# Kernel tuning notes

Hardware: AMD Instinct MI355X
Metric: run time of the kernel (lower is better)

The kernel has to match this reference:

```python
import jax, jax.numpy as jnp
import numpy as np


def setup_inputs() -> dict:
    key = jax.random.key(0)
    k1, k2 = jax.random.split(key)
    x = jax.random.normal(k1, (32, 64, 64, 64), dtype=jnp.float32)
    codebook = jax.random.normal(k2, (1024, 64), dtype=jnp.float32)
    return {"x": x, "codebook": codebook}


def reference(x, codebook):
    # x: (B, D, H, W)  codebook: (K, D)
    B, D = x.shape[0], x.shape[1]
    spatial = x.shape[2:]
    flat = x.reshape(B, D, -1).transpose(0, 2, 1)  # (B, N, D)
    dot = jnp.einsum("bnd,kd->bnk", flat, codebook)
    cb_norm = jnp.sum(codebook * codebook, axis=-1)  # (K,)
    indices = jnp.argmin(cb_norm[None, None, :] - 2.0 * dot, axis=-1)  # (B, N)
    quantized = codebook[indices]  # (B, N, D) gather
    out = quantized.transpose(0, 2, 1).reshape(x.shape)
    return out, indices.reshape((B,) + spatial)
```

## Files before the change

### kernel.cpp

```cpp
#include <hip/hip_runtime.h>


typedef _Float16 f16x8 __attribute__((ext_vector_type(8)));
typedef float    f32x4 __attribute__((ext_vector_type(4)));

#define VQ_D    64
#define VQ_HW   4096
#define VQ_NPOS 131072
#define SC      2048.0f
#define ISC     (1.0f / 2048.0f)
#define EPS     2.0e-3f
#define WS_CBN  65536
#define WS_CBT  66560
#define WS_CNT  132096
#define WS_LIST 132100

__global__ __launch_bounds__(256)
void vq_prep(const float* __restrict__ cb, float* __restrict__ ws)
{
    const int tid = threadIdx.x;
    const int blk = blockIdx.x;
    if (blk < 64) {
        const int it   = blk * 256 + tid;
        const int ct   = it >> 8;
        const int s    = (it >> 6) & 3;
        const int lane = it & 63;
        const int ks   = s & 1, isR = s >> 1;
        const int n    = ct * 16 + (lane & 15);
        const int k0   = ks * 32 + (lane >> 4) * 8;
        const float* src = cb + n * 64 + k0;
        f16x8 o;
        #pragma unroll
        for (int j = 0; j < 8; ++j) {
            const float b = src[j];
            const _Float16 bh = (_Float16)b;
            o[j] = isR ? (_Float16)((b - (float)bh) * (-2.0f * SC))
                       : (_Float16)(-2.0f * (float)bh);
        }
        ((f16x8*)ws)[it] = o;
    } else if (blk < 128) {
        const int it = (blk - 64) * 256 + tid;
        const int k = it >> 4, j4 = it & 15;
        ((float4*)(ws + WS_CBT))[j4 * 1024 + k] = ((const float4*)cb)[it];
    } else {
        const int k = (blk - 128) * 256 + tid;
        const float4* row = (const float4*)(cb + k * 64);
        float a0 = 0.f, a1 = 0.f, a2 = 0.f, a3 = 0.f;
        #pragma unroll
        for (int j = 0; j < 16; ++j) {
            const float4 c = row[j];
            a0 = fmaf(c.x, c.x, a0); a1 = fmaf(c.y, c.y, a1);
            a2 = fmaf(c.z, c.z, a2); a3 = fmaf(c.w, c.w, a3);
        }
        ws[WS_CBN + k] = (a0 + a1) + (a2 + a3);
        if (k == 0) ((int*)ws)[WS_CNT] = 0;
    }
}

#define PREFETCH(B0, B1, R0, R1, CV, CTN)                          \
    {                                                              \
        const f16x8* base_ = bp + (CTN) * 256;                     \
        B0 = base_[lane];       B1 = base_[64 + lane];             \
        R0 = base_[128 + lane]; R1 = base_[192 + lane];            \
        CV = cnb[(CTN) * 16 + m];                                  \
    }

#define COMPUTE(B0, B1, R0, R1, CV, CTV)                                                   \
    {                                                                                      \
        const f32x4 Ci = {CV, CV, CV, CV};                                                 \
        f32x4 acm[4], acc[4];                                                              \
        _Pragma("unroll")                                                                  \
        for (int tl = 0; tl < 4; ++tl) {                                                   \
            acm[tl] = __builtin_amdgcn_mfma_f32_16x16x32_f16(Ah[tl][0], B0, Ci,      0,0,0);\
            acm[tl] = __builtin_amdgcn_mfma_f32_16x16x32_f16(Ah[tl][1], B1, acm[tl], 0,0,0);\
            acc[tl] = __builtin_amdgcn_mfma_f32_16x16x32_f16(Ah[tl][0], R0, zero4,   0,0,0);\
            acc[tl] = __builtin_amdgcn_mfma_f32_16x16x32_f16(Ah[tl][1], R1, acc[tl], 0,0,0);\
            acc[tl] = __builtin_amdgcn_mfma_f32_16x16x32_f16(Ra[tl][0], B0, acc[tl], 0,0,0);\
            acc[tl] = __builtin_amdgcn_mfma_f32_16x16x32_f16(Ra[tl][1], B1, acc[tl], 0,0,0);\
        }                                                                                  \
        const int code_ = (CTV) * 16 + m;                                                  \
        _Pragma("unroll")                                                                  \
        for (int tl = 0; tl < 4; ++tl)                                                     \
            _Pragma("unroll")                                                              \
            for (int r = 0; r < 4; ++r) {                                                  \
                const float dist = fmaf(acc[tl][r], ISC, acm[tl][r]);                      \
                const float od   = d1[tl][r];                                              \
                const bool  c    = dist < od;                                              \
                d2[tl][r] = __builtin_amdgcn_fmed3f(dist, od, d2[tl][r]);                  \
                d1[tl][r] = c ? dist : od;                                                 \
                k1[tl][r] = c ? code_ : k1[tl][r];                                         \
            }                                                                              \
    }

__global__ __launch_bounds__(256, 2)
void vq_main(const float* __restrict__ x,
             const float* __restrict__ cb,
             float* __restrict__ ws,
             float* __restrict__ out,
             float* __restrict__ idx_out)
{
    __shared__ int   sk[256];
    __shared__ float smg[256];

    const int tid  = threadIdx.x;
    const int lane = tid & 63;
    const int wv   = tid >> 6;
    const int m    = lane & 15;
    const int q    = lane >> 4;

    const f16x8* bp  = (const f16x8*)ws;
    const float* cnb = ws + WS_CBN;

    const int p0 = blockIdx.x * 256;
    const int b  = p0 >> 12;
    const int n0 = p0 & (VQ_HW - 1);
    const float* xw = x + (size_t)b * (VQ_D * VQ_HW) + n0 + wv * 64;

    f16x8 Ah[4][2], Ra[4][2];
    #pragma unroll
    for (int tl = 0; tl < 4; ++tl)
        #pragma unroll
        for (int ks = 0; ks < 2; ++ks) {
            f16x8 h8, r8;
            #pragma unroll
            for (int j = 0; j < 8; ++j) {
                const int k = ks * 32 + q * 8 + j;
                const float v = xw[(size_t)k * VQ_HW + tl * 16 + m];
                const _Float16 vh = (_Float16)v;
                h8[j] = vh;
                r8[j] = (_Float16)((v - (float)vh) * SC);
            }
            Ah[tl][ks] = h8; Ra[tl][ks] = r8;
        }

    float d1[4][4], d2[4][4]; int k1[4][4];
    #pragma unroll
    for (int tl = 0; tl < 4; ++tl)
        #pragma unroll
        for (int r = 0; r < 4; ++r) { d1[tl][r] = 3.4e38f; d2[tl][r] = 3.4e38f; k1[tl][r] = 0; }

    const f32x4 zero4 = {0.f, 0.f, 0.f, 0.f};

    f16x8 B0a, B1a, R0a, R1a, B0b, B1b, R0b, R1b;
    float cva, cvb;
    PREFETCH(B0a, B1a, R0a, R1a, cva, 0)
    PREFETCH(B0b, B1b, R0b, R1b, cvb, 1)

    for (int ct = 0; ct < 64; ct += 2) {
        COMPUTE(B0a, B1a, R0a, R1a, cva, ct)
        {
            const int ctn = (ct + 2 < 64) ? ct + 2 : 62;
            PREFETCH(B0a, B1a, R0a, R1a, cva, ctn)
        }
        COMPUTE(B0b, B1b, R0b, R1b, cvb, ct + 1)
        {
            const int ctn = (ct + 3 < 64) ? ct + 3 : 63;
            PREFETCH(B0b, B1b, R0b, R1b, cvb, ctn)
        }
    }

    #pragma unroll
    for (int off = 1; off < 16; off <<= 1)
        #pragma unroll
        for (int tl = 0; tl < 4; ++tl)
            #pragma unroll
            for (int r = 0; r < 4; ++r) {
                const float od1 = __shfl_xor(d1[tl][r], off, 64);
                const float od2 = __shfl_xor(d2[tl][r], off, 64);
                const int   ok1 = __shfl_xor(k1[tl][r], off, 64);
                const float nd2 = fminf(fmaxf(d1[tl][r], od1), fminf(d2[tl][r], od2));
                const bool  sw  = (od1 < d1[tl][r]) ||
                                  (od1 == d1[tl][r] && ok1 < k1[tl][r]);
                d1[tl][r] = sw ? od1 : d1[tl][r];
                k1[tl][r] = sw ? ok1 : k1[tl][r];
                d2[tl][r] = nd2;
            }

    if (m == 0) {
        #pragma unroll
        for (int tl = 0; tl < 4; ++tl)
            #pragma unroll
            for (int r = 0; r < 4; ++r) {
                const int li = wv * 64 + tl * 16 + q * 4 + r;
                sk[li]  = k1[tl][r];
                smg[li] = d2[tl][r] - d1[tl][r];
            }
    }
    __syncthreads();

    idx_out[p0 + tid] = (float)sk[tid];
    if (smg[tid] < EPS) {
        const int slot = atomicAdd((int*)ws + WS_CNT, 1);
        ((int*)ws)[WS_LIST + slot] = p0 + tid;
    }
    const int bk = sk[tid];
    const float4* cr = (const float4*)(cb + (size_t)bk * VQ_D);
    float* ob = out + (size_t)b * (VQ_D * VQ_HW) + n0 + tid;
    #pragma unroll
    for (int d4 = 0; d4 < 16; ++d4) {
        const float4 v = cr[d4];
        ob[(size_t)(d4 * 4 + 0) * VQ_HW] = v.x;
        ob[(size_t)(d4 * 4 + 1) * VQ_HW] = v.y;
        ob[(size_t)(d4 * 4 + 2) * VQ_HW] = v.z;
        ob[(size_t)(d4 * 4 + 3) * VQ_HW] = v.w;
    }
}

__global__ __launch_bounds__(64)
void vq_rescan(const float* __restrict__ x,
               const float* __restrict__ cb,
               const float* __restrict__ ws,
               float* __restrict__ out,
               float* __restrict__ idx_out)
{
    __shared__ float xs[VQ_D];
    const int lane = threadIdx.x;
    const int cnt  = ((const int*)ws)[WS_CNT];
    const int* list = (const int*)ws + WS_LIST;
    const float*  cnb  = ws + WS_CBN;
    const float4* cbT4 = (const float4*)(ws + WS_CBT);

    for (int i = blockIdx.x; i < cnt; i += gridDim.x) {
        const int p = list[i];
        const int b = p >> 12, n = p & (VQ_HW - 1);
        xs[lane] = x[(size_t)b * (VQ_D * VQ_HW) + (size_t)lane * VQ_HW + n];
        __syncthreads();
        float4 xr[16];
        #pragma unroll
        for (int j = 0; j < 16; ++j) xr[j] = ((const float4*)xs)[j];

        float bd = 3.4e38f; int bk = 0;
        #pragma unroll 4
        for (int t = 0; t < 16; ++t) {
            const int code = t * 64 + lane;
            float a0 = 0.f, a1 = 0.f, a2 = 0.f, a3 = 0.f;
            #pragma unroll
            for (int j4 = 0; j4 < 16; ++j4) {
                const float4 c = cbT4[j4 * 1024 + code];
                a0 = fmaf(xr[j4].x, c.x, a0); a1 = fmaf(xr[j4].y, c.y, a1);
                a2 = fmaf(xr[j4].z, c.z, a2); a3 = fmaf(xr[j4].w, c.w, a3);
            }
            const float dist = fmaf(-2.0f, (a0 + a1) + (a2 + a3), cnb[code]);
            if (dist < bd) { bd = dist; bk = code; }
        }
        #pragma unroll
        for (int off = 1; off < 64; off <<= 1) {
            const float od = __shfl_xor(bd, off, 64);
            const int   ok = __shfl_xor(bk, off, 64);
            if (od < bd || (od == bd && ok < bk)) { bd = od; bk = ok; }
        }
        out[(size_t)b * (VQ_D * VQ_HW) + (size_t)lane * VQ_HW + n] = cb[(size_t)bk * VQ_D + lane];
        if (lane == 0) idx_out[p] = (float)bk;
        __syncthreads();
    }
}

extern "C" void kernel_launch(void* const* d_in, const int* in_sizes, int n_in,
                              void* d_out, int out_size, void* d_ws, size_t ws_size,
                              hipStream_t stream) {
    const float* x  = (const float*)d_in[0];
    const float* cb = (const float*)d_in[1];
    float* out = (float*)d_out;
    float* idx = out + (size_t)VQ_NPOS * VQ_D;
    float* ws  = (float*)d_ws;

    vq_prep  <<<dim3(132),  dim3(256), 0, stream>>>(cb, ws);
    vq_main  <<<dim3(512),  dim3(256), 0, stream>>>(x, cb, ws, out, idx);
    vq_rescan<<<dim3(1024), dim3(64),  0, stream>>>(x, cb, ws, out, idx);
}
```

Before: 162.4 us.

## Use single fp16 MFMA pass with packed index, LDS-staged codebook, wider rescan

Drops the split-fp16 residual MFMAs, so the main kernel computes distances with one fp16 product per codebook tile. The code index is packed into the low mantissa bits so argmin reduces to plain fminf. Codebook tiles are staged through double-buffered LDS, and blocks shrink to 128 positions with higher occupancy. The looser approximation is covered by raising the rescan margin from 2e-3 to 1.0 and launching more rescan blocks, which risks many more positions falling to the slow exact rescan.

```diff
diff --git a/kernel.cpp b/kernel.cpp
--- a/kernel.cpp
+++ b/kernel.cpp
@@ -7,9 +7,7 @@
 #define VQ_D    64
 #define VQ_HW   4096
 #define VQ_NPOS 131072
-#define SC      2048.0f
-#define ISC     (1.0f / 2048.0f)
-#define EPS     2.0e-3f
+#define EPS     1.0f
 #define WS_CBN  65536
 #define WS_CBT  66560
 #define WS_CNT  132096
@@ -20,30 +18,25 @@
 {
     const int tid = threadIdx.x;
     const int blk = blockIdx.x;
-    if (blk < 64) {
+    if (blk < 32) {
         const int it   = blk * 256 + tid;
-        const int ct   = it >> 8;
-        const int s    = (it >> 6) & 3;
+        const int ct   = it >> 7;
+        const int s    = (it >> 6) & 1;
         const int lane = it & 63;
-        const int ks   = s & 1, isR = s >> 1;
         const int n    = ct * 16 + (lane & 15);
-        const int k0   = ks * 32 + (lane >> 4) * 8;
+        const int k0   = s * 32 + (lane >> 4) * 8;
         const float* src = cb + n * 64 + k0;
         f16x8 o;
         #pragma unroll
-        for (int j = 0; j < 8; ++j) {
-            const float b = src[j];
-            const _Float16 bh = (_Float16)b;
-            o[j] = isR ? (_Float16)((b - (float)bh) * (-2.0f * SC))
-                       : (_Float16)(-2.0f * (float)bh);
-        }
+        for (int j = 0; j < 8; ++j)
+            o[j] = (_Float16)(-2.0f * (float)(_Float16)src[j]);
         ((f16x8*)ws)[it] = o;
-    } else if (blk < 128) {
-        const int it = (blk - 64) * 256 + tid;
+    } else if (blk < 96) {
+        const int it = (blk - 32) * 256 + tid;
         const int k = it >> 4, j4 = it & 15;
         ((float4*)(ws + WS_CBT))[j4 * 1024 + k] = ((const float4*)cb)[it];
     } else {
-        const int k = (blk - 128) * 256 + tid;
+        const int k = (blk - 96) * 256 + tid;
         const float4* row = (const float4*)(cb + k * 64);
         float a0 = 0.f, a1 = 0.f, a2 = 0.f, a3 = 0.f;
         #pragma unroll
@@ -57,50 +50,17 @@
     }
 }
 
-#define PREFETCH(B0, B1, R0, R1, CV, CTN)                          \
-    {                                                              \
-        const f16x8* base_ = bp + (CTN) * 256;                     \
-        B0 = base_[lane];       B1 = base_[64 + lane];             \
-        R0 = base_[128 + lane]; R1 = base_[192 + lane];            \
-        CV = cnb[(CTN) * 16 + m];                                  \
-    }
-
-#define COMPUTE(B0, B1, R0, R1, CV, CTV)                                                   \
-    {                                                                                      \
-        const f32x4 Ci = {CV, CV, CV, CV};                                                 \
-        f32x4 acm[4], acc[4];                                                              \
-        _Pragma("unroll")                                                                  \
-        for (int tl = 0; tl < 4; ++tl) {                                                   \
-            acm[tl] = __builtin_amdgcn_mfma_f32_16x16x32_f16(Ah[tl][0], B0, Ci,      0,0,0);\
-            acm[tl] = __builtin_amdgcn_mfma_f32_16x16x32_f16(Ah[tl][1], B1, acm[tl], 0,0,0);\
-            acc[tl] = __builtin_amdgcn_mfma_f32_16x16x32_f16(Ah[tl][0], R0, zero4,   0,0,0);\
-            acc[tl] = __builtin_amdgcn_mfma_f32_16x16x32_f16(Ah[tl][1], R1, acc[tl], 0,0,0);\
-            acc[tl] = __builtin_amdgcn_mfma_f32_16x16x32_f16(Ra[tl][0], B0, acc[tl], 0,0,0);\
-            acc[tl] = __builtin_amdgcn_mfma_f32_16x16x32_f16(Ra[tl][1], B1, acc[tl], 0,0,0);\
-        }                                                                                  \
-        const int code_ = (CTV) * 16 + m;                                                  \
-        _Pragma("unroll")                                                                  \
-        for (int tl = 0; tl < 4; ++tl)                                                     \
-            _Pragma("unroll")                                                              \
-            for (int r = 0; r < 4; ++r) {                                                  \
-                const float dist = fmaf(acc[tl][r], ISC, acm[tl][r]);                      \
-                const float od   = d1[tl][r];                                              \
-                const bool  c    = dist < od;                                              \
-                d2[tl][r] = __builtin_amdgcn_fmed3f(dist, od, d2[tl][r]);                  \
-                d1[tl][r] = c ? dist : od;                                                 \
-                k1[tl][r] = c ? code_ : k1[tl][r];                                         \
-            }                                                                              \
-    }
-
-__global__ __launch_bounds__(256, 2)
+__global__ __launch_bounds__(256, 4)
 void vq_main(const float* __restrict__ x,
              const float* __restrict__ cb,
              float* __restrict__ ws,
              float* __restrict__ out,
              float* __restrict__ idx_out)
 {
-    __shared__ int   sk[256];
-    __shared__ float smg[256];
+    __shared__ f16x8 bbuf[2][1024];
+    __shared__ float cn_lds[1024];
+    __shared__ int   sk[128];
+    __shared__ float smg[128];
 
     const int tid  = threadIdx.x;
     const int lane = tid & 63;
@@ -108,96 +68,113 @@
     const int m    = lane & 15;
     const int q    = lane >> 4;
 
-    const f16x8* bp  = (const f16x8*)ws;
-    const float* cnb = ws + WS_CBN;
-
-    const int p0 = blockIdx.x * 256;
+    const int p0 = blockIdx.x * 128;
     const int b  = p0 >> 12;
     const int n0 = p0 & (VQ_HW - 1);
-    const float* xw = x + (size_t)b * (VQ_D * VQ_HW) + n0 + wv * 64;
-
-    f16x8 Ah[4][2], Ra[4][2];
-    #pragma unroll
-    for (int tl = 0; tl < 4; ++tl)
+    const float* xw = x + (size_t)b * (VQ_D * VQ_HW) + n0 + wv * 32;
+
+    ((float4*)cn_lds)[tid] = ((const float4*)(ws + WS_CBN))[tid];
+
+    const float4* g0 = (const float4*)ws;
+    float4 u0 = g0[tid], u1 = g0[256 + tid], u2 = g0[512 + tid], u3 = g0[768 + tid];
+
+    f16x8 Ah[2][2];
+    #pragma unroll
+    for (int tl = 0; tl < 2; ++tl)
         #pragma unroll
         for (int ks = 0; ks < 2; ++ks) {
-            f16x8 h8, r8;
-            #pragma unroll
-            for (int j = 0; j < 8; ++j) {
-                const int k = ks * 32 + q * 8 + j;
-                const float v = xw[(size_t)k * VQ_HW + tl * 16 + m];
-                const _Float16 vh = (_Float16)v;
-                h8[j] = vh;
-                r8[j] = (_Float16)((v - (float)vh) * SC);
-            }
-            Ah[tl][ks] = h8; Ra[tl][ks] = r8;
-        }
-
-    float d1[4][4], d2[4][4]; int k1[4][4];
-    #pragma unroll
-    for (int tl = 0; tl < 4; ++tl)
-        #pragma unroll
-        for (int r = 0; r < 4; ++r) { d1[tl][r] = 3.4e38f; d2[tl][r] = 3.4e38f; k1[tl][r] = 0; }
-
-    const f32x4 zero4 = {0.f, 0.f, 0.f, 0.f};
-
-    f16x8 B0a, B1a, R0a, R1a, B0b, B1b, R0b, R1b;
-    float cva, cvb;
-    PREFETCH(B0a, B1a, R0a, R1a, cva, 0)
-    PREFETCH(B0b, B1b, R0b, R1b, cvb, 1)
-
-    for (int ct = 0; ct < 64; ct += 2) {
-        COMPUTE(B0a, B1a, R0a, R1a, cva, ct)
-        {
-            const int ctn = (ct + 2 < 64) ? ct + 2 : 62;
-            PREFETCH(B0a, B1a, R0a, R1a, cva, ctn)
-        }
-        COMPUTE(B0b, B1b, R0b, R1b, cvb, ct + 1)
-        {
-            const int ctn = (ct + 3 < 64) ? ct + 3 : 63;
-            PREFETCH(B0b, B1b, R0b, R1b, cvb, ctn)
+            f16x8 h8;
+            #pragma unroll
+            for (int j = 0; j < 8; ++j)
+                h8[j] = (_Float16)xw[(size_t)(ks * 32 + q * 8 + j) * VQ_HW + tl * 16 + m];
+            Ah[tl][ks] = h8;
+        }
+
+    {
+        float4* l0 = (float4*)(&bbuf[0][0]);
+        l0[tid] = u0; l0[256 + tid] = u1; l0[512 + tid] = u2; l0[768 + tid] = u3;
+    }
+
+    float d1[2][4], d2[2][4];
+    #pragma unroll
+    for (int tl = 0; tl < 2; ++tl)
+        #pragma unroll
+        for (int r = 0; r < 4; ++r) { d1[tl][r] = 3.4e38f; d2[tl][r] = 3.4e38f; }
+
+    for (int cc = 0; cc < 8; ++cc) {
+        __syncthreads();
+        float4 t0, t1, t2, t3;
+        if (cc < 7) {
+            const float4* g = (const float4*)((const char*)ws + (size_t)(cc + 1) * 16384);
+            t0 = g[tid]; t1 = g[256 + tid]; t2 = g[512 + tid]; t3 = g[768 + tid];
+        }
+        const f16x8* bufc = &bbuf[cc & 1][0];
+        #pragma unroll
+        for (int ct = 0; ct < 8; ++ct) {
+            const int ctg = cc * 8 + ct;
+            const f16x8 B0 = bufc[ct * 128 + lane];
+            const f16x8 B1 = bufc[ct * 128 + 64 + lane];
+            const float cv = cn_lds[ctg * 16 + m];
+            const f32x4 Ci = {cv, cv, cv, cv};
+            f32x4 a0 = __builtin_amdgcn_mfma_f32_16x16x32_f16(Ah[0][0], B0, Ci, 0, 0, 0);
+            a0       = __builtin_amdgcn_mfma_f32_16x16x32_f16(Ah[0][1], B1, a0, 0, 0, 0);
+            f32x4 a1 = __builtin_amdgcn_mfma_f32_16x16x32_f16(Ah[1][0], B0, Ci, 0, 0, 0);
+            a1       = __builtin_amdgcn_mfma_f32_16x16x32_f16(Ah[1][1], B1, a1, 0, 0, 0);
+            const int code_ = ctg * 16 + m;
+            #pragma unroll
+            for (int r = 0; r < 4; ++r) {
+                const float kf0 = __int_as_float((int)((__float_as_int(a0[r]) & 0xFFFFFC00u) | (unsigned)code_));
+                d2[0][r] = __builtin_amdgcn_fmed3f(kf0, d1[0][r], d2[0][r]);
+                d1[0][r] = fminf(kf0, d1[0][r]);
+                const float kf1 = __int_as_float((int)((__float_as_int(a1[r]) & 0xFFFFFC00u) | (unsigned)code_));
+                d2[1][r] = __builtin_amdgcn_fmed3f(kf1, d1[1][r], d2[1][r]);
+                d1[1][r] = fminf(kf1, d1[1][r]);
+            }
+        }
+        if (cc < 7) {
+            float4* l = (float4*)(&bbuf[(cc + 1) & 1][0]);
+            l[tid] = t0; l[256 + tid] = t1; l[512 + tid] = t2; l[768 + tid] = t3;
         }
     }
 
     #pragma unroll
     for (int off = 1; off < 16; off <<= 1)
         #pragma unroll
-        for (int tl = 0; tl < 4; ++tl)
+        for (int tl = 0; tl < 2; ++tl)
             #pragma unroll
             for (int r = 0; r < 4; ++r) {
                 const float od1 = __shfl_xor(d1[tl][r], off, 64);
                 const float od2 = __shfl_xor(d2[tl][r], off, 64);
-                const int   ok1 = __shfl_xor(k1[tl][r], off, 64);
-                const float nd2 = fminf(fmaxf(d1[tl][r], od1), fminf(d2[tl][r], od2));
-                const bool  sw  = (od1 < d1[tl][r]) ||
-                                  (od1 == d1[tl][r] && ok1 < k1[tl][r]);
-                d1[tl][r] = sw ? od1 : d1[tl][r];
-                k1[tl][r] = sw ? ok1 : k1[tl][r];
-                d2[tl][r] = nd2;
+                d2[tl][r] = fminf(fmaxf(d1[tl][r], od1), fminf(d2[tl][r], od2));
+                d1[tl][r] = fminf(d1[tl][r], od1);
             }
 
     if (m == 0) {
         #pragma unroll
-        for (int tl = 0; tl < 4; ++tl)
+        for (int tl = 0; tl < 2; ++tl)
             #pragma unroll
             for (int r = 0; r < 4; ++r) {
-                const int li = wv * 64 + tl * 16 + q * 4 + r;
-                sk[li]  = k1[tl][r];
+                const int li = wv * 32 + tl * 16 + q * 4 + r;
+                sk[li]  = __float_as_int(d1[tl][r]) & 1023;
                 smg[li] = d2[tl][r] - d1[tl][r];
             }
     }
     __syncthreads();
 
-    idx_out[p0 + tid] = (float)sk[tid];
-    if (smg[tid] < EPS) {
-        const int slot = atomicAdd((int*)ws + WS_CNT, 1);
-        ((int*)ws)[WS_LIST + slot] = p0 + tid;
-    }
-    const int bk = sk[tid];
-    const float4* cr = (const float4*)(cb + (size_t)bk * VQ_D);
-    float* ob = out + (size_t)b * (VQ_D * VQ_HW) + n0 + tid;
-    #pragma unroll
-    for (int d4 = 0; d4 < 16; ++d4) {
+    const int pos  = tid & 127;
+    const int half = tid >> 7;
+    const int bk   = sk[pos];
+    if (half == 0) {
+        idx_out[p0 + pos] = (float)bk;
+        if (smg[pos] < EPS) {
+            const int slot = atomicAdd((int*)ws + WS_CNT, 1);
+            ((int*)ws)[WS_LIST + slot] = p0 + pos;
+        }
+    }
+    const float4* cr = (const float4*)(cb + (size_t)bk * VQ_D) + half * 8;
+    float* ob = out + (size_t)b * (VQ_D * VQ_HW) + (size_t)(half * 32) * VQ_HW + n0 + pos;
+    #pragma unroll
+    for (int d4 = 0; d4 < 8; ++d4) {
         const float4 v = cr[d4];
         ob[(size_t)(d4 * 4 + 0) * VQ_HW] = v.x;
         ob[(size_t)(d4 * 4 + 1) * VQ_HW] = v.y;
@@ -264,7 +241,7 @@
     float* idx = out + (size_t)VQ_NPOS * VQ_D;
     float* ws  = (float*)d_ws;
 
-    vq_prep  <<<dim3(132),  dim3(256), 0, stream>>>(cb, ws);
-    vq_main  <<<dim3(512),  dim3(256), 0, stream>>>(x, cb, ws, out, idx);
-    vq_rescan<<<dim3(1024), dim3(64),  0, stream>>>(x, cb, ws, out, idx);
-}
+    vq_prep  <<<dim3(100),  dim3(256), 0, stream>>>(cb, ws);
+    vq_main  <<<dim3(1024), dim3(256), 0, stream>>>(x, cb, ws, out, idx);
+    vq_rescan<<<dim3(4096), dim3(64),  0, stream>>>(x, cb, ws, out, idx);
+}
```

New measurement: 407.3 us. 2.51x slower.
